# Performance work log

Measured on AMD Instinct MI355X. Metric: run time of the kernel, lower is better.

The kernel has to match this reference:

```python
import jax, jax.numpy as jnp
import numpy as np

N_NODES = 50000
N_EDGES = 1600000
IN_DIM = 128
HEADS = 2
OUT_CH = 32
NEG_SLOPE = 0.2


def setup_inputs() -> dict:
    key = jax.random.key(0)
    k1, k2, k3, k4, k5, k6 = jax.random.split(key, 6)
    x = jax.random.normal(k1, (N_NODES, IN_DIM), dtype=jnp.float32)
    # Glorot-ish scale for weights
    W = jax.random.normal(k2, (IN_DIM, HEADS * OUT_CH), dtype=jnp.float32) * (1.0 / np.sqrt(IN_DIM))
    att_src = jax.random.normal(k3, (HEADS, OUT_CH), dtype=jnp.float32) * (1.0 / np.sqrt(OUT_CH))
    att_dst = jax.random.normal(k4, (HEADS, OUT_CH), dtype=jnp.float32) * (1.0 / np.sqrt(OUT_CH))
    bias = jnp.zeros((HEADS * OUT_CH,), dtype=jnp.float32)
    edge_index = jax.random.randint(k5, (2, N_EDGES), 0, N_NODES, dtype=jnp.int32)
    return {"x": x, "W": W, "att_src": att_src, "att_dst": att_dst,
            "bias": bias, "edge_index": edge_index}


def reference(x, W, att_src, att_dst, bias, edge_index):
    N = x.shape[0]
    # ELU on input features (IntraGraphAttention.forward)
    xf = jax.nn.elu(x)
    # Shared linear projection, per-head view: [N, H, C]
    h = (xf @ W).reshape(N, HEADS, OUT_CH)
    # add_self_loops=True (PyG GATConv default)
    loops = jnp.arange(N, dtype=edge_index.dtype)
    src = jnp.concatenate([edge_index[0], loops])
    dst = jnp.concatenate([edge_index[1], loops])
    # Per-node attention halves: [N, H]
    a_src = jnp.einsum('nhc,hc->nh', h, att_src)
    a_dst = jnp.einsum('nhc,hc->nh', h, att_dst)
    # Per-edge logits with leaky relu: [E, H]
    logits = a_src[src] + a_dst[dst]
    logits = jnp.where(logits >= 0, logits, NEG_SLOPE * logits)
    # Segment softmax over incoming edges of each dst node
    seg_max = jax.ops.segment_max(logits, dst, num_segments=N)
    e = jnp.exp(logits - seg_max[dst])
    denom = jax.ops.segment_sum(e, dst, num_segments=N)
    alpha = e / (denom[dst] + 1e-16)  # [E, H]
    # Weighted scatter-aggregate of source features: [N, H, C]
    msgs = h[src] * alpha[:, :, None]
    out = jax.ops.segment_sum(msgs, dst, num_segments=N)
    # concat=True -> [N, H*C], plus bias
    return out.reshape(N, HEADS * OUT_CH) + bias
```

## Files before the change

### kernel.cpp

```cpp
#include <hip/hip_runtime.h>
#include <hip/hip_bf16.h>

#define NN 50000
#define EE 1600000

__device__ __forceinline__ float bflo(unsigned u) { return __uint_as_float(u << 16); }
__device__ __forceinline__ float bfhi(unsigned u) { return __uint_as_float(u & 0xffff0000u); }

__global__ __launch_bounds__(256) void k_proj(
    const float* __restrict__ x, const float* __restrict__ W,
    const float* __restrict__ att_src, const float* __restrict__ att_dst,
    unsigned short* __restrict__ h2, float* __restrict__ a_src, float* __restrict__ a_dst) {
  __shared__ float Wl[128 * 64];
  __shared__ float xs[16 * 128];
  int tid = threadIdx.x;
  for (int i = tid; i < 128 * 64; i += 256) Wl[i] = W[i];
  int row0 = blockIdx.x * 16;
  for (int i = tid; i < 16 * 128; i += 256) {
    float v = x[row0 * 128 + i];
    xs[i] = v > 0.f ? v : (__expf(v) - 1.f);
  }
  __syncthreads();
  int w = tid >> 6, c = tid & 63;
  float acc[4] = {0.f, 0.f, 0.f, 0.f};
#pragma unroll 4
  for (int k = 0; k < 128; ++k) {
    float wv = Wl[k * 64 + c];
#pragma unroll
    for (int j = 0; j < 4; ++j) acc[j] += xs[(w * 4 + j) * 128 + k] * wv;
  }
  int hh = c >> 5, cc = c & 31;
  float asv = att_src[hh * 32 + cc], adv = att_dst[hh * 32 + cc];
#pragma unroll
  for (int j = 0; j < 4; ++j) {
    int row = row0 + w * 4 + j;
    h2[row * 64 + c] = __bfloat16_as_ushort(__float2bfloat16(acc[j]));
    float ps = acc[j] * asv, pd = acc[j] * adv;
#pragma unroll
    for (int o = 16; o > 0; o >>= 1) {
      ps += __shfl_xor(ps, o);
      pd += __shfl_xor(pd, o);
    }
    if (cc == 0) { a_src[row * 2 + hh] = ps; a_dst[row * 2 + hh] = pd; }
  }
}

__global__ __launch_bounds__(256) void k_build(const int* __restrict__ dst,
                                               int* __restrict__ headA,
                                               int* __restrict__ nxt) {
  int e = blockIdx.x * 256 + threadIdx.x;
  int d = dst[e];
  int old = atomicExch(&headA[d * 4 + (e & 3)], e);
  nxt[e] = old;
}

__global__ __launch_bounds__(256) void k_agg(
    const unsigned* __restrict__ h2u, const float* __restrict__ a_src,
    const float* __restrict__ a_dst, const int* __restrict__ headA,
    const int* __restrict__ nxt, const int* __restrict__ srcv,
    const float* __restrict__ bias, float* __restrict__ out) {
  int n = blockIdx.x * 4 + (threadIdx.x >> 6);
  int lane = threadIdx.x & 63;
  int c2 = lane & 31;
  int half = lane >> 5;
  int hh = c2 >> 4;
  float ad = a_dst[n * 2 + hh];

  float denom, acc0, acc1;
  if (half == 0) {
    float l0 = a_src[n * 2 + hh] + ad;
    l0 = fmaxf(l0, 0.2f * l0);
    float es = __expf(l0);
    unsigned hv = h2u[n * 32 + c2];
    denom = es; acc0 = es * bflo(hv); acc1 = es * bfhi(hv);
  } else {
    denom = 0.f; acc0 = 0.f; acc1 = 0.f;
  }

  int eA = headA[n * 4 + 2 * half];
  int eB = headA[n * 4 + 2 * half + 1];
  while (__any(max(eA, eB) >= 0)) {
    int iA = max(eA, 0), iB = max(eB, 0);
    int sA = srcv[iA], sB = srcv[iB];
    int nA = nxt[iA],  nB = nxt[iB];
    unsigned hA = h2u[sA * 32 + c2], hB = h2u[sB * 32 + c2];
    float aA = a_src[sA * 2 + hh],  aB = a_src[sB * 2 + hh];
    float lA = aA + ad; lA = fmaxf(lA, 0.2f * lA);
    float lB = aB + ad; lB = fmaxf(lB, 0.2f * lB);
    float xA = (eA >= 0) ? __expf(lA) : 0.f;
    float xB = (eB >= 0) ? __expf(lB) : 0.f;
    denom += xA + xB;
    acc0 += xA * bflo(hA) + xB * bflo(hB);
    acc1 += xA * bfhi(hA) + xB * bfhi(hB);
    eA = (eA >= 0) ? nA : -1;
    eB = (eB >= 0) ? nB : -1;
  }
  denom += __shfl_xor(denom, 32);
  acc0  += __shfl_xor(acc0, 32);
  acc1  += __shfl_xor(acc1, 32);
  if (half == 0) {
    float inv = 1.f / (denom + 1e-16f);
    float2 b = ((const float2*)bias)[c2];
    float2 o;
    o.x = acc0 * inv + b.x;
    o.y = acc1 * inv + b.y;
    ((float2*)out)[n * 32 + c2] = o;
  }
}

extern "C" void kernel_launch(void* const* d_in, const int* in_sizes, int n_in,
                              void* d_out, int out_size, void* d_ws, size_t ws_size,
                              hipStream_t stream) {
  const float* x       = (const float*)d_in[0];
  const float* W       = (const float*)d_in[1];
  const float* att_src = (const float*)d_in[2];
  const float* att_dst = (const float*)d_in[3];
  const float* bias    = (const float*)d_in[4];
  const int* edge_index = (const int*)d_in[5];
  const int* esrc = edge_index;
  const int* edst = edge_index + EE;

  char* base = (char*)d_ws;
  unsigned short* h2 = (unsigned short*)base;
  float* a_src_b = (float*)(base + 6400000);
  float* a_dst_b = (float*)(base + 6800000);
  int*   headA   = (int*)(base + 7200000);
  int*   nxt     = (int*)(base + 8000000);

  hipMemsetAsync(headA, 0xFF, 200000 * sizeof(int), stream);
  k_proj<<<NN / 16, 256, 0, stream>>>(x, W, att_src, att_dst, h2, a_src_b, a_dst_b);
  k_build<<<EE / 256, 256, 0, stream>>>(edst, headA, nxt);
  k_agg<<<NN / 4, 256, 0, stream>>>((const unsigned*)h2, a_src_b, a_dst_b, headA,
                                    nxt, esrc, bias, (float*)d_out);
}
```

Measured before the change: 264.5 us.

## Interleave src/next edge records and use eight parallel linked-list chains

The edge build now stores each edge's source index and next pointer together as one int2 record. The per-destination head array grows from 4 to 8 chains, so each half-wavefront walks 4 independent chains per iteration instead of 2. This shortens the dependent pointer-chasing latency chain and halves the number of separate gathers per edge. The projection kernel also processes 32 rows per block, with each thread computing two adjacent channels, a padded shared tile and packed bf16 stores. The cost is a larger head memset, more registers in the aggregation loop, and more wasted lanes when chains have uneven lengths.

```diff
diff --git a/kernel.cpp b/kernel.cpp
--- a/kernel.cpp
+++ b/kernel.cpp
@@ -10,55 +10,72 @@
 __global__ __launch_bounds__(256) void k_proj(
     const float* __restrict__ x, const float* __restrict__ W,
     const float* __restrict__ att_src, const float* __restrict__ att_dst,
-    unsigned short* __restrict__ h2, float* __restrict__ a_src, float* __restrict__ a_dst) {
+    unsigned* __restrict__ h2u, float* __restrict__ a_src, float* __restrict__ a_dst) {
   __shared__ float Wl[128 * 64];
-  __shared__ float xs[16 * 128];
+  __shared__ float xs[32 * 129];
   int tid = threadIdx.x;
+  int row0 = blockIdx.x * 32;
   for (int i = tid; i < 128 * 64; i += 256) Wl[i] = W[i];
-  int row0 = blockIdx.x * 16;
-  for (int i = tid; i < 16 * 128; i += 256) {
-    float v = x[row0 * 128 + i];
-    xs[i] = v > 0.f ? v : (__expf(v) - 1.f);
+  for (int i = tid; i < 32 * 128; i += 256) {
+    int r = i >> 7, k = i & 127;
+    int row = row0 + r;
+    float v = (row < NN) ? x[row * 128 + k] : 0.f;
+    xs[r * 129 + k] = v > 0.f ? v : (__expf(v) - 1.f);
   }
   __syncthreads();
-  int w = tid >> 6, c = tid & 63;
-  float acc[4] = {0.f, 0.f, 0.f, 0.f};
+  int w = tid >> 6, lane = tid & 63;
+  int rs = lane >> 5, c = lane & 31;
+  int rbase = w * 8 + rs * 4;
+  float a0[4] = {0, 0, 0, 0}, a1[4] = {0, 0, 0, 0};
+  const float2* W2 = (const float2*)Wl;
 #pragma unroll 4
   for (int k = 0; k < 128; ++k) {
-    float wv = Wl[k * 64 + c];
+    float2 wv = W2[k * 32 + c];
 #pragma unroll
-    for (int j = 0; j < 4; ++j) acc[j] += xs[(w * 4 + j) * 128 + k] * wv;
+    for (int j = 0; j < 4; ++j) {
+      float xv = xs[(rbase + j) * 129 + k];
+      a0[j] += xv * wv.x;
+      a1[j] += xv * wv.y;
+    }
   }
-  int hh = c >> 5, cc = c & 31;
-  float asv = att_src[hh * 32 + cc], adv = att_dst[hh * 32 + cc];
+  int hh = c >> 4;
+  float2 av_s = ((const float2*)att_src)[c];
+  float2 av_d = ((const float2*)att_dst)[c];
 #pragma unroll
   for (int j = 0; j < 4; ++j) {
-    int row = row0 + w * 4 + j;
-    h2[row * 64 + c] = __bfloat16_as_ushort(__float2bfloat16(acc[j]));
-    float ps = acc[j] * asv, pd = acc[j] * adv;
+    int row = row0 + rbase + j;
+    bool ok = row < NN;
+    if (ok) {
+      unsigned lo = (unsigned)__bfloat16_as_ushort(__float2bfloat16(a0[j]));
+      unsigned hi = (unsigned)__bfloat16_as_ushort(__float2bfloat16(a1[j]));
+      h2u[row * 32 + c] = lo | (hi << 16);
+    }
+    float ps = a0[j] * av_s.x + a1[j] * av_s.y;
+    float pd = a0[j] * av_d.x + a1[j] * av_d.y;
 #pragma unroll
-    for (int o = 16; o > 0; o >>= 1) {
+    for (int o = 1; o < 16; o <<= 1) {
       ps += __shfl_xor(ps, o);
       pd += __shfl_xor(pd, o);
     }
-    if (cc == 0) { a_src[row * 2 + hh] = ps; a_dst[row * 2 + hh] = pd; }
+    if (ok && (c & 15) == 0) { a_src[row * 2 + hh] = ps; a_dst[row * 2 + hh] = pd; }
   }
 }
 
-__global__ __launch_bounds__(256) void k_build(const int* __restrict__ dst,
-                                               int* __restrict__ headA,
-                                               int* __restrict__ nxt) {
+__global__ __launch_bounds__(256) void k_build(const int* __restrict__ src,
+                                               const int* __restrict__ dst,
+                                               int* __restrict__ head8,
+                                               int2* __restrict__ edge2) {
   int e = blockIdx.x * 256 + threadIdx.x;
   int d = dst[e];
-  int old = atomicExch(&headA[d * 4 + (e & 3)], e);
-  nxt[e] = old;
+  int old = atomicExch(&head8[d * 8 + (e & 7)], e);
+  edge2[e] = make_int2(src[e], old);
 }
 
 __global__ __launch_bounds__(256) void k_agg(
     const unsigned* __restrict__ h2u, const float* __restrict__ a_src,
-    const float* __restrict__ a_dst, const int* __restrict__ headA,
-    const int* __restrict__ nxt, const int* __restrict__ srcv,
-    const float* __restrict__ bias, float* __restrict__ out) {
+    const float* __restrict__ a_dst, const int* __restrict__ head8,
+    const int2* __restrict__ edge2, const float* __restrict__ bias,
+    float* __restrict__ out) {
   int n = blockIdx.x * 4 + (threadIdx.x >> 6);
   int lane = threadIdx.x & 63;
   int c2 = lane & 31;
@@ -66,34 +83,40 @@
   int hh = c2 >> 4;
   float ad = a_dst[n * 2 + hh];
 
-  float denom, acc0, acc1;
+  float denom = 0.f, acc0 = 0.f, acc1 = 0.f;
   if (half == 0) {
     float l0 = a_src[n * 2 + hh] + ad;
     l0 = fmaxf(l0, 0.2f * l0);
     float es = __expf(l0);
     unsigned hv = h2u[n * 32 + c2];
     denom = es; acc0 = es * bflo(hv); acc1 = es * bfhi(hv);
-  } else {
-    denom = 0.f; acc0 = 0.f; acc1 = 0.f;
   }
 
-  int eA = headA[n * 4 + 2 * half];
-  int eB = headA[n * 4 + 2 * half + 1];
-  while (__any(max(eA, eB) >= 0)) {
-    int iA = max(eA, 0), iB = max(eB, 0);
-    int sA = srcv[iA], sB = srcv[iB];
-    int nA = nxt[iA],  nB = nxt[iB];
-    unsigned hA = h2u[sA * 32 + c2], hB = h2u[sB * 32 + c2];
-    float aA = a_src[sA * 2 + hh],  aB = a_src[sB * 2 + hh];
-    float lA = aA + ad; lA = fmaxf(lA, 0.2f * lA);
-    float lB = aB + ad; lB = fmaxf(lB, 0.2f * lB);
-    float xA = (eA >= 0) ? __expf(lA) : 0.f;
-    float xB = (eB >= 0) ? __expf(lB) : 0.f;
-    denom += xA + xB;
-    acc0 += xA * bflo(hA) + xB * bflo(hB);
-    acc1 += xA * bfhi(hA) + xB * bfhi(hB);
-    eA = (eA >= 0) ? nA : -1;
-    eB = (eB >= 0) ? nB : -1;
+  int e0 = head8[n * 8 + half * 4 + 0];
+  int e1 = head8[n * 8 + half * 4 + 1];
+  int e2 = head8[n * 8 + half * 4 + 2];
+  int e3 = head8[n * 8 + half * 4 + 3];
+  while (__any(max(max(e0, e1), max(e2, e3)) >= 0)) {
+    int2 p0 = edge2[max(e0, 0)];
+    int2 p1 = edge2[max(e1, 0)];
+    int2 p2 = edge2[max(e2, 0)];
+    int2 p3 = edge2[max(e3, 0)];
+    unsigned h0 = h2u[p0.x * 32 + c2], h1 = h2u[p1.x * 32 + c2];
+    unsigned h2 = h2u[p2.x * 32 + c2], h3 = h2u[p3.x * 32 + c2];
+    float A0 = a_src[p0.x * 2 + hh], A1 = a_src[p1.x * 2 + hh];
+    float A2 = a_src[p2.x * 2 + hh], A3 = a_src[p3.x * 2 + hh];
+    float l;
+    l = A0 + ad; l = fmaxf(l, 0.2f * l); float x0 = (e0 >= 0) ? __expf(l) : 0.f;
+    l = A1 + ad; l = fmaxf(l, 0.2f * l); float x1 = (e1 >= 0) ? __expf(l) : 0.f;
+    l = A2 + ad; l = fmaxf(l, 0.2f * l); float x2 = (e2 >= 0) ? __expf(l) : 0.f;
+    l = A3 + ad; l = fmaxf(l, 0.2f * l); float x3 = (e3 >= 0) ? __expf(l) : 0.f;
+    denom += (x0 + x1) + (x2 + x3);
+    acc0 += x0 * bflo(h0) + x1 * bflo(h1) + x2 * bflo(h2) + x3 * bflo(h3);
+    acc1 += x0 * bfhi(h0) + x1 * bfhi(h1) + x2 * bfhi(h2) + x3 * bfhi(h3);
+    e0 = (e0 >= 0) ? p0.y : -1;
+    e1 = (e1 >= 0) ? p1.y : -1;
+    e2 = (e2 >= 0) ? p2.y : -1;
+    e3 = (e3 >= 0) ? p3.y : -1;
   }
   denom += __shfl_xor(denom, 32);
   acc0  += __shfl_xor(acc0, 32);
@@ -101,10 +124,7 @@
   if (half == 0) {
     float inv = 1.f / (denom + 1e-16f);
     float2 b = ((const float2*)bias)[c2];
-    float2 o;
-    o.x = acc0 * inv + b.x;
-    o.y = acc1 * inv + b.y;
-    ((float2*)out)[n * 32 + c2] = o;
+    ((float2*)out)[n * 32 + c2] = make_float2(acc0 * inv + b.x, acc1 * inv + b.y);
   }
 }
 
@@ -121,15 +141,16 @@
   const int* edst = edge_index + EE;
 
   char* base = (char*)d_ws;
-  unsigned short* h2 = (unsigned short*)base;
+  unsigned* h2u  = (unsigned*)base;
   float* a_src_b = (float*)(base + 6400000);
   float* a_dst_b = (float*)(base + 6800000);
-  int*   headA   = (int*)(base + 7200000);
-  int*   nxt     = (int*)(base + 8000000);
+  int*   head8   = (int*)(base + 7200000);
+  int2*  edge2   = (int2*)(base + 8800000);
 
-  hipMemsetAsync(headA, 0xFF, 200000 * sizeof(int), stream);
-  k_proj<<<NN / 16, 256, 0, stream>>>(x, W, att_src, att_dst, h2, a_src_b, a_dst_b);
-  k_build<<<EE / 256, 256, 0, stream>>>(edst, headA, nxt);
-  k_agg<<<NN / 4, 256, 0, stream>>>((const unsigned*)h2, a_src_b, a_dst_b, headA,
-                                    nxt, esrc, bias, (float*)d_out);
+  hipMemsetAsync(head8, 0xFF, 400000 * sizeof(int), stream);
+  k_proj<<<(NN + 31) / 32, 256, 0, stream>>>(x, W, att_src, att_dst, h2u,
+                                             a_src_b, a_dst_b);
+  k_build<<<EE / 256, 256, 0, stream>>>(esrc, edst, head8, edge2);
+  k_agg<<<NN / 4, 256, 0, stream>>>(h2u, a_src_b, a_dst_b, head8, edge2, bias,
+                                    (float*)d_out);
 }
```

New measurement: 262.0 us. Within noise of the previous version (-1.0%).
